# Kernel tuning notes

Hardware: AMD Instinct MI355X
Metric: run time of the kernel (lower is better)

The kernel has to match this reference:

```python
import jax, jax.numpy as jnp
import numpy as np

B, N, C, H = 4, 2048, 768, 12
D = C // H  # 64
EPS = 1e-12


def setup_inputs() -> dict:
    key = jax.random.key(0)
    ks = jax.random.split(key, 8)
    s = 0.02
    return {
        "x": jax.random.normal(ks[0], (B, N, C), dtype=jnp.float32),
        "Wq": jax.random.normal(ks[1], (C, C), dtype=jnp.float32) * s,
        "bq": jnp.zeros((C,), dtype=jnp.float32),
        "Wkv": jax.random.normal(ks[2], (C, 2 * C), dtype=jnp.float32) * s,
        "bkv": jnp.zeros((2 * C,), dtype=jnp.float32),
        "Wproj": jax.random.normal(ks[3], (C, C), dtype=jnp.float32) * s,
        "bproj": jnp.zeros((C,), dtype=jnp.float32),
        "scale": jnp.full((1, H, 1, 1), D ** -0.5, dtype=jnp.float32),
    }


def _l2norm(t):
    # F.normalize(dim=-1): x / max(||x||_2, eps)
    n = jnp.sqrt(jnp.sum(t * t, axis=-1, keepdims=True))
    return t / jnp.maximum(n, EPS)


def reference(x, Wq, bq, Wkv, bkv, Wproj, bproj, scale):
    b, n, c = x.shape
    q = (x @ Wq + bq).reshape(b, n, H, D).transpose(0, 2, 1, 3)        # [B,H,N,D]
    kv = (x @ Wkv + bkv).reshape(b, n, 2, H, D).transpose(2, 0, 3, 1, 4)
    k, v = kv[0], kv[1]                                                # [B,H,N,D]
    q = _l2norm(q)
    k = _l2norm(k)
    attn = jnp.einsum("bhqd,bhkd->bhqk", q, k) * scale                 # [B,H,N,N]
    attn = jax.nn.softmax(attn, axis=-1)
    out = jnp.einsum("bhqk,bhkd->bhqd", attn, v)                       # [B,H,N,D]
    out = out.transpose(0, 2, 1, 3).reshape(b, n, c)
    return out @ Wproj + bproj
```

## Files before the change

kernel.cpp:

```cpp
#include <hip/hip_runtime.h>
#include <hip/hip_bf16.h>
#include <math.h>


typedef short bf16x8 __attribute__((ext_vector_type(8)));
typedef float f32x4 __attribute__((ext_vector_type(4)));
typedef float f32x16 __attribute__((ext_vector_type(16)));

static __device__ __forceinline__ unsigned short f2bf(float f) {
    unsigned int u = __float_as_uint(f);
    unsigned int r = u + 0x7fff + ((u >> 16) & 1);
    return (unsigned short)(r >> 16);
}
static __device__ __forceinline__ unsigned int pack2(float a, float b) {
    return (unsigned int)f2bf(a) | ((unsigned int)f2bf(b) << 16);
}
static __device__ __forceinline__ unsigned int cvtpk(float a, float b) {
    unsigned int r;
    asm("v_cvt_pk_bf16_f32 %0, %1, %2" : "=v"(r) : "v"(a), "v"(b));
    return r;
}
static __device__ __forceinline__ void gl_lds16(const void* g, void* l) {
    __builtin_amdgcn_global_load_lds(
        (const __attribute__((address_space(1))) unsigned int*)g,
        (__attribute__((address_space(3))) unsigned int*)l, 16, 0, 0);
}

__global__ __launch_bounds__(256) void convx_kernel(
    const float* __restrict__ in, unsigned short* __restrict__ out)
{
    size_t i = ((size_t)blockIdx.x * 256 + threadIdx.x) * 8;
    float4 a = *(const float4*)&in[i];
    float4 b = *(const float4*)&in[i + 4];
    uint4 o = make_uint4(pack2(a.x, a.y), pack2(a.z, a.w), pack2(b.x, b.y), pack2(b.z, b.w));
    *(uint4*)&out[i] = o;
}

__global__ __launch_bounds__(256) void convT_kernel(
    const float* __restrict__ Wq, const float* __restrict__ Wkv, const float* __restrict__ Wp,
    unsigned short* __restrict__ WqkvT, unsigned short* __restrict__ WprjT)
{
    __shared__ char tb[8192];
    const int bx = blockIdx.x, k0 = blockIdx.y * 64;
    const float* src; int ld; int cbase; unsigned short* out; int c0;
    if (bx < 36) {
        c0 = bx * 64; out = WqkvT;
        if (c0 < 768) { src = Wq;  ld = 768;  cbase = c0; }
        else          { src = Wkv; ld = 1536; cbase = c0 - 768; }
    } else {
        c0 = (bx - 36) * 64; out = WprjT; src = Wp; ld = 768; cbase = c0;
    }
    const int t = threadIdx.x;
    const int kl = t >> 2, cq = (t & 3) * 16;
    #pragma unroll
    for (int jj = 0; jj < 4; ++jj) {
        float4 v = *(const float4*)&src[(size_t)(k0 + kl) * ld + cbase + cq + jj * 4];
        float vv[4] = {v.x, v.y, v.z, v.w};
        #pragma unroll
        for (int je = 0; je < 4; ++je) {
            int c = cq + jj * 4 + je;
            *(unsigned short*)(tb + c * 128 + ((kl * 2) ^ ((c & 7) << 4))) = f2bf(vv[je]);
        }
    }
    __syncthreads();
    const int cl = t >> 2, u2 = (t & 3) * 2;
    uint4 r0 = *(const uint4*)(tb + cl * 128 + ((u2 ^ (cl & 7)) << 4));
    uint4 r1 = *(const uint4*)(tb + cl * 128 + (((u2 + 1) ^ (cl & 7)) << 4));
    size_t ob = (size_t)(c0 + cl) * 768 + k0 + (t & 3) * 16;
    *(uint4*)&out[ob] = r0;
    *(uint4*)&out[ob + 8] = r1;
}

__global__ __launch_bounds__(256) void qkv_gemm_kernel(
    const unsigned short* __restrict__ xb, const unsigned short* __restrict__ WT,
    const float* __restrict__ bq, const float* __restrict__ bkv,
    const float* __restrict__ scale,
    unsigned short* __restrict__ Qb, unsigned short* __restrict__ Kb,
    unsigned short* __restrict__ Vtb)
{
    __shared__ char lds[32768] __attribute__((aligned(16)));

    const int ct = blockIdx.x;
    const int row0 = blockIdx.y * 128;
    const int tid = threadIdx.x;
    const int w = tid >> 6, l = tid & 63;
    const int g = l >> 4, ln = l & 15;
    const int wr = w >> 1, wc = w & 1;
    const int col0 = ct * 128;

    const int srow = (w & 1) * 64 + (l >> 3);
    const int su = ((l & 7) ^ (l >> 3)) * 16;
    const char* s = (w < 2)
        ? (const char*)xb + (size_t)(row0 + srow) * 1536 + su
        : (const char*)WT + (size_t)(col0 + srow) * 1536 + su;
    char* dbase = lds + ((w >= 2) ? 16384 : 0) + (w & 1) * 8192;

    f32x4 acc[4][4];
    #pragma unroll
    for (int m = 0; m < 4; ++m)
        #pragma unroll
        for (int n = 0; n < 4; ++n) acc[m][n] = (f32x4){0.f, 0.f, 0.f, 0.f};

    const int arow = (wr * 64 + ln) * 128;
    const int brow = 16384 + (wc * 64 + ln) * 128;
    const int x0 = ((0 + g) ^ (ln & 7)) * 16;
    const int x1 = ((4 + g) ^ (ln & 7)) * 16;

    for (int ks = 0; ks < 12; ++ks) {
        __syncthreads();
        #pragma unroll
        for (int j = 0; j < 8; ++j)
            gl_lds16(s + (size_t)j * 8 * 1536, dbase + j * 1024);
        s += 128;
        __syncthreads();
        #pragma unroll
        for (int kc = 0; kc < 2; ++kc) {
            const int xo = kc ? x1 : x0;
            bf16x8 af[4], bfr[4];
            #pragma unroll
            for (int m = 0; m < 4; ++m) af[m] = *(const bf16x8*)(lds + arow + m * 2048 + xo);
            #pragma unroll
            for (int n = 0; n < 4; ++n) bfr[n] = *(const bf16x8*)(lds + brow + n * 2048 + xo);
            #pragma unroll
            for (int m = 0; m < 4; ++m)
                #pragma unroll
                for (int n = 0; n < 4; ++n)
                    acc[m][n] = __builtin_amdgcn_mfma_f32_16x16x32_bf16(af[m], bfr[n], acc[m][n], 0, 0, 0);
        }
    }

    const int co = col0 + wc * 64 + ln;
    float bv[4];
    #pragma unroll
    for (int n = 0; n < 4; ++n) {
        int c = co + n * 16;
        bv[n] = (c < 768) ? bq[c] : bkv[c - 768];
    }
    const int region = ct / 6;
    const int h = (ct % 6) * 2 + wc;

    if (region < 2) {
        unsigned short* dst = (region == 0) ? Qb : Kb;
        const float post = (region == 0) ? scale[0] * 1.4426950408889634f : 1.0f;
        #pragma unroll
        for (int m = 0; m < 4; ++m) {
            #pragma unroll
            for (int n = 0; n < 4; ++n)
                #pragma unroll
                for (int r = 0; r < 4; ++r) acc[m][n][r] += bv[n];
            #pragma unroll
            for (int r = 0; r < 4; ++r) {
                float ss = 0.f;
                #pragma unroll
                for (int n = 0; n < 4; ++n) ss += acc[m][n][r] * acc[m][n][r];
                ss += __shfl_xor(ss, 1); ss += __shfl_xor(ss, 2);
                ss += __shfl_xor(ss, 4); ss += __shfl_xor(ss, 8);
                float inv = post / fmaxf(sqrtf(ss), 1e-12f);
                int t = row0 + wr * 64 + m * 16 + g * 4 + r;
                int b = t >> 11, nt = t & 2047;
                size_t base = ((size_t)(b * 12 + h) * 2048 + nt) * 64 + ln;
                #pragma unroll
                for (int n = 0; n < 4; ++n)
                    dst[base + n * 16] = f2bf(acc[m][n][r] * inv);
            }
        }
    } else {
        char* tb = lds + w * 8192;
        __syncthreads();
        #pragma unroll
        for (int m = 0; m < 4; ++m)
            #pragma unroll
            for (int n = 0; n < 4; ++n)
                #pragma unroll
                for (int r = 0; r < 4; ++r) {
                    int d = n * 16 + ln;
                    int tok = m * 16 + g * 4 + r;
                    *(unsigned short*)(tb + d * 128 + ((tok * 2) ^ ((d & 7) << 4))) =
                        f2bf(acc[m][n][r] + bv[n]);
                }
        __syncthreads();
        const int t0 = row0 + wr * 64;
        const int b = t0 >> 11, n0 = t0 & 2047;
        #pragma unroll
        for (int i = 0; i < 8; ++i) {
            int d = i * 8 + (l >> 3);
            uint4 v = *(const uint4*)(tb + d * 128 + (((l & 7) ^ (d & 7)) << 4));
            *(uint4*)&Vtb[((size_t)(b * 12 + h) * 64 + d) * 2048 + n0 + (l & 7) * 8] = v;
        }
    }
}

__global__ __launch_bounds__(128, 2) void attn_kernel(
    const unsigned short* __restrict__ Qg, const unsigned short* __restrict__ Kg,
    const unsigned short* __restrict__ Vtg,
    unsigned short* __restrict__ O)
{
    __shared__ char lds[32768] __attribute__((aligned(16)));

    const int bid = blockIdx.y * 16 + blockIdx.x;
    const int swzb = (bid & 7) * 96 + (bid >> 3);
    const int bh = swzb >> 4;
    const int q0 = (swzb & 15) * 128;

    const int tid = threadIdx.x;
    const int w  = tid >> 6;
    const int l  = tid & 63;
    const int lo = l & 31;
    const int hi = l >> 5;

    const int srow = w * 32 + (l >> 3);
    const int su   = ((l & 7) ^ (l >> 3)) * 16;
    const char* kS = (const char*)Kg  + ((size_t)bh * 2048 + srow) * 128 + su;
    const char* vS = (const char*)Vtg + ((size_t)bh * 64   + srow) * 4096 + su;
    char* kD = lds + w * 4096;
    char* vD = lds + 16384 + w * 4096;

    auto stage = [&](int t, int buf) {
        const char* pk = kS + (size_t)t * 8192;
        const char* pv = vS + (size_t)t * 128;
        char* dk = kD + buf * 8192;
        char* dv = vD + buf * 8192;
        #pragma unroll
        for (int i = 0; i < 4; ++i) {
            gl_lds16(pk + i * 1024, dk + i * 1024);
            gl_lds16(pv + (size_t)i * 32768, dv + i * 1024);
        }
    };

    bf16x8 qfA[4], qfB[4];
    {
        const unsigned short* qp = Qg + ((size_t)bh * 2048 + q0 + w * 64 + lo) * 64 + hi * 8;
        #pragma unroll
        for (int c = 0; c < 4; ++c) {
            qfA[c] = *(const bf16x8*)(qp + c * 16);
            qfB[c] = *(const bf16x8*)(qp + 2048 + c * 16);
        }
    }

    const int swz = (lo & 7) << 4;
    const int rowb = lo * 128;
    int coff[4];
    #pragma unroll
    for (int c = 0; c < 4; ++c) coff[c] = (c * 32 + hi * 16) ^ swz;

    f32x16 oA0, oA1, oB0, oB1;
    #pragma unroll
    for (int r = 0; r < 16; ++r) { oA0[r] = 0.f; oA1[r] = 0.f; oB0[r] = 0.f; oB1[r] = 0.f; }
    float rsA = 0.f, rsB = 0.f;

    const f32x16 zero16 = {0.f,0.f,0.f,0.f,0.f,0.f,0.f,0.f,0.f,0.f,0.f,0.f,0.f,0.f,0.f,0.f};

    auto compute = [&](const int OFF) {
        const char* Kb = lds + OFF;
        const char* Vb = lds + 16384 + OFF;

        bf16x8 kf[4], kg2[4];
        #pragma unroll
        for (int c = 0; c < 4; ++c) {
            kf[c]  = *(const bf16x8*)(Kb + rowb + coff[c]);
            kg2[c] = *(const bf16x8*)(Kb + 4096 + rowb + coff[c]);
        }

        f32x16 sA0, sA1, sB0, sB1;
        __builtin_amdgcn_s_setprio(1);
        sA0 = __builtin_amdgcn_mfma_f32_32x32x16_bf16(kf[0], qfA[0], zero16, 0, 0, 0);
        sA0 = __builtin_amdgcn_mfma_f32_32x32x16_bf16(kf[1], qfA[1], sA0, 0, 0, 0);
        sA0 = __builtin_amdgcn_mfma_f32_32x32x16_bf16(kf[2], qfA[2], sA0, 0, 0, 0);
        sA0 = __builtin_amdgcn_mfma_f32_32x32x16_bf16(kf[3], qfA[3], sA0, 0, 0, 0);
        sA1 = __builtin_amdgcn_mfma_f32_32x32x16_bf16(kg2[0], qfA[0], zero16, 0, 0, 0);
        sA1 = __builtin_amdgcn_mfma_f32_32x32x16_bf16(kg2[1], qfA[1], sA1, 0, 0, 0);
        sA1 = __builtin_amdgcn_mfma_f32_32x32x16_bf16(kg2[2], qfA[2], sA1, 0, 0, 0);
        sA1 = __builtin_amdgcn_mfma_f32_32x32x16_bf16(kg2[3], qfA[3], sA1, 0, 0, 0);
        sB0 = __builtin_amdgcn_mfma_f32_32x32x16_bf16(kf[0], qfB[0], zero16, 0, 0, 0);
        sB0 = __builtin_amdgcn_mfma_f32_32x32x16_bf16(kf[1], qfB[1], sB0, 0, 0, 0);
        sB0 = __builtin_amdgcn_mfma_f32_32x32x16_bf16(kf[2], qfB[2], sB0, 0, 0, 0);
        sB0 = __builtin_amdgcn_mfma_f32_32x32x16_bf16(kf[3], qfB[3], sB0, 0, 0, 0);
        sB1 = __builtin_amdgcn_mfma_f32_32x32x16_bf16(kg2[0], qfB[0], zero16, 0, 0, 0);
        sB1 = __builtin_amdgcn_mfma_f32_32x32x16_bf16(kg2[1], qfB[1], sB1, 0, 0, 0);
        sB1 = __builtin_amdgcn_mfma_f32_32x32x16_bf16(kg2[2], qfB[2], sB1, 0, 0, 0);
        sB1 = __builtin_amdgcn_mfma_f32_32x32x16_bf16(kg2[3], qfB[3], sB1, 0, 0, 0);
        __builtin_amdgcn_s_setprio(0);

        unsigned int pA[16], pB[16];
        #pragma unroll
        for (int kb = 0; kb < 2; ++kb) {
            float e[16];
            #pragma unroll
            for (int r = 0; r < 16; ++r)
                e[r] = __builtin_amdgcn_exp2f(kb ? sA1[r] : sA0[r]);
            float t = 0.f;
            #pragma unroll
            for (int r = 0; r < 16; r += 4) t += (e[r] + e[r+1]) + (e[r+2] + e[r+3]);
            rsA += t;
            #pragma unroll
            for (int ksb = 0; ksb < 2; ++ksb) {
                pA[kb*8 + ksb*4 + 0] = cvtpk(e[ksb*8 + 0], e[ksb*8 + 1]);
                pA[kb*8 + ksb*4 + 1] = cvtpk(e[ksb*8 + 2], e[ksb*8 + 3]);
                pA[kb*8 + ksb*4 + 2] = cvtpk(e[ksb*8 + 4], e[ksb*8 + 5]);
                pA[kb*8 + ksb*4 + 3] = cvtpk(e[ksb*8 + 6], e[ksb*8 + 7]);
            }
        }
        #pragma unroll
        for (int kb = 0; kb < 2; ++kb) {
            float e[16];
            #pragma unroll
            for (int r = 0; r < 16; ++r)
                e[r] = __builtin_amdgcn_exp2f(kb ? sB1[r] : sB0[r]);
            float t = 0.f;
            #pragma unroll
            for (int r = 0; r < 16; r += 4) t += (e[r] + e[r+1]) + (e[r+2] + e[r+3]);
            rsB += t;
            #pragma unroll
            for (int ksb = 0; ksb < 2; ++ksb) {
                pB[kb*8 + ksb*4 + 0] = cvtpk(e[ksb*8 + 0], e[ksb*8 + 1]);
                pB[kb*8 + ksb*4 + 1] = cvtpk(e[ksb*8 + 2], e[ksb*8 + 3]);
                pB[kb*8 + ksb*4 + 2] = cvtpk(e[ksb*8 + 4], e[ksb*8 + 5]);
                pB[kb*8 + ksb*4 + 3] = cvtpk(e[ksb*8 + 6], e[ksb*8 + 7]);
            }
        }

        #pragma unroll
        for (int kb = 0; kb < 2; ++kb) {
            #pragma unroll
            for (int ksb = 0; ksb < 2; ++ksb) {
                const int base = kb*8 + ksb*4;
                const int ks = kb*2 + ksb;
                bf16x8 v0 = *(const bf16x8*)(Vb + rowb + coff[ks]);
                bf16x8 v1 = *(const bf16x8*)(Vb + 4096 + rowb + coff[ks]);
                unsigned int a0 = pA[base], a1 = pA[base+1], a2 = pA[base+2], a3 = pA[base+3];
                asm("v_permlane32_swap_b32 %0, %1" : "+v"(a0), "+v"(a2));
                asm("v_permlane32_swap_b32 %0, %1" : "+v"(a1), "+v"(a3));
                unsigned int fwA[4] = {a0, a1, a2, a3};
                bf16x8 paA; __builtin_memcpy(&paA, fwA, 16);
                unsigned int b0 = pB[base], b1 = pB[base+1], b2 = pB[base+2], b3 = pB[base+3];
                asm("v_permlane32_swap_b32 %0, %1" : "+v"(b0), "+v"(b2));
                asm("v_permlane32_swap_b32 %0, %1" : "+v"(b1), "+v"(b3));
                unsigned int fwB[4] = {b0, b1, b2, b3};
                bf16x8 paB; __builtin_memcpy(&paB, fwB, 16);
                __builtin_amdgcn_s_setprio(1);
                oA0 = __builtin_amdgcn_mfma_f32_32x32x16_bf16(paA, v0, oA0, 0, 0, 0);
                oA1 = __builtin_amdgcn_mfma_f32_32x32x16_bf16(paA, v1, oA1, 0, 0, 0);
                oB0 = __builtin_amdgcn_mfma_f32_32x32x16_bf16(paB, v0, oB0, 0, 0, 0);
                oB1 = __builtin_amdgcn_mfma_f32_32x32x16_bf16(paB, v1, oB1, 0, 0, 0);
                __builtin_amdgcn_s_setprio(0);
            }
        }
    };

    stage(0, 0);
    __syncthreads();

    #pragma unroll 1
    for (int it = 0; it < 16; ++it) {
        stage(2 * it + 1, 1);
        compute(0);
        __syncthreads();
        if (it < 15) stage(2 * it + 2, 0);
        compute(8192);
        __syncthreads();
    }

    float vA = rsA; vA += __shfl_xor(vA, 32);
    float vB = rsB; vB += __shfl_xor(vB, 32);
    const int b = bh / 12, h = bh % 12;
    #pragma unroll
    for (int r = 0; r < 16; ++r) {
        const int qr = (r & 3) + 8 * (r >> 2) + 4 * hi;
        float invA = 1.0f / __shfl(vA, qr);
        float invB = 1.0f / __shfl(vB, qr);
        size_t baseA = ((size_t)(b * 2048 + q0 + w * 64 + qr)) * 768 + h * 64 + lo;
        O[baseA]      = f2bf(oA0[r] * invA);
        O[baseA + 32] = f2bf(oA1[r] * invA);
        size_t baseB = baseA + (size_t)32 * 768;
        O[baseB]      = f2bf(oB0[r] * invB);
        O[baseB + 32] = f2bf(oB1[r] * invB);
    }
}

__global__ __launch_bounds__(256) void proj_gemm_kernel(
    const unsigned short* __restrict__ Ob, const unsigned short* __restrict__ WT,
    const float* __restrict__ bp, float* __restrict__ out)
{
    __shared__ char lds[32768] __attribute__((aligned(16)));

    const int row0 = blockIdx.y * 128;
    const int col0 = blockIdx.x * 128;
    const int tid = threadIdx.x;
    const int w = tid >> 6, l = tid & 63;
    const int g = l >> 4, ln = l & 15;
    const int wr = w >> 1, wc = w & 1;

    const int srow = (w & 1) * 64 + (l >> 3);
    const int su = ((l & 7) ^ (l >> 3)) * 16;
    const char* s = (w < 2)
        ? (const char*)Ob + (size_t)(row0 + srow) * 1536 + su
        : (const char*)WT + (size_t)(col0 + srow) * 1536 + su;
    char* dbase = lds + ((w >= 2) ? 16384 : 0) + (w & 1) * 8192;

    f32x4 acc[4][4];
    #pragma unroll
    for (int m = 0; m < 4; ++m)
        #pragma unroll
        for (int n = 0; n < 4; ++n) acc[m][n] = (f32x4){0.f, 0.f, 0.f, 0.f};

    const int arow = (wr * 64 + ln) * 128;
    const int brow = 16384 + (wc * 64 + ln) * 128;
    const int x0 = ((0 + g) ^ (ln & 7)) * 16;
    const int x1 = ((4 + g) ^ (ln & 7)) * 16;

    for (int ks = 0; ks < 12; ++ks) {
        __syncthreads();
        #pragma unroll
        for (int j = 0; j < 8; ++j)
            gl_lds16(s + (size_t)j * 8 * 1536, dbase + j * 1024);
        s += 128;
        __syncthreads();
        #pragma unroll
        for (int kc = 0; kc < 2; ++kc) {
            const int xo = kc ? x1 : x0;
            bf16x8 af[4], bfr[4];
            #pragma unroll
            for (int m = 0; m < 4; ++m) af[m] = *(const bf16x8*)(lds + arow + m * 2048 + xo);
            #pragma unroll
            for (int n = 0; n < 4; ++n) bfr[n] = *(const bf16x8*)(lds + brow + n * 2048 + xo);
            #pragma unroll
            for (int m = 0; m < 4; ++m)
                #pragma unroll
                for (int n = 0; n < 4; ++n)
                    acc[m][n] = __builtin_amdgcn_mfma_f32_16x16x32_bf16(af[m], bfr[n], acc[m][n], 0, 0, 0);
        }
    }

    const int co = col0 + wc * 64 + ln;
    float bv[4];
    #pragma unroll
    for (int n = 0; n < 4; ++n) bv[n] = bp[co + n * 16];
    #pragma unroll
    for (int m = 0; m < 4; ++m)
        #pragma unroll
        for (int r = 0; r < 4; ++r) {
            int t = row0 + wr * 64 + m * 16 + g * 4 + r;
            #pragma unroll
            for (int n = 0; n < 4; ++n)
                out[(size_t)t * 768 + co + n * 16] = acc[m][n][r] + bv[n];
        }
}

extern "C" void kernel_launch(void* const* d_in, const int* in_sizes, int n_in,
                              void* d_out, int out_size, void* d_ws, size_t ws_size,
                              hipStream_t stream) {
    const float* x     = (const float*)d_in[0];
    const float* Wq    = (const float*)d_in[1];
    const float* bq    = (const float*)d_in[2];
    const float* Wkv   = (const float*)d_in[3];
    const float* bkv   = (const float*)d_in[4];
    const float* Wp    = (const float*)d_in[5];
    const float* bp    = (const float*)d_in[6];
    const float* scale = (const float*)d_in[7];
    float* out = (float*)d_out;

    unsigned short* ws = (unsigned short*)d_ws;
    const size_t SZ = (size_t)4 * 12 * 2048 * 64;
    unsigned short* xbw   = ws;
    unsigned short* WqkvT = xbw + SZ;
    unsigned short* WprjT = WqkvT + (size_t)2304 * 768;
    unsigned short* Qw    = WprjT + (size_t)768 * 768;
    unsigned short* Kw    = Qw + SZ;
    unsigned short* Vtw   = Kw + SZ;
    unsigned short* Ow    = Vtw + SZ;

    convx_kernel<<<3072, 256, 0, stream>>>(x, xbw);
    convT_kernel<<<dim3(48, 12), 256, 0, stream>>>(Wq, Wkv, Wp, WqkvT, WprjT);
    qkv_gemm_kernel<<<dim3(18, 64), 256, 0, stream>>>(xbw, WqkvT, bq, bkv, scale, Qw, Kw, Vtw);
    attn_kernel<<<dim3(16, 48), 128, 0, stream>>>(Qw, Kw, Vtw, Ow);
    proj_gemm_kernel<<<dim3(6, 64), 256, 0, stream>>>(Ow, WprjT, bp, out);
}
```

Before: 148.5 us.

## Split attention key tiles across two waves per query group with LDS reduction

New measurement: 163.9 us. +10.4%, slower.

```diff
diff --git a/kernel.cpp b/kernel.cpp
--- a/kernel.cpp
+++ b/kernel.cpp
@@ -190,12 +190,12 @@
     }
 }
 
-__global__ __launch_bounds__(128, 2) void attn_kernel(
+__global__ __launch_bounds__(256, 3) void attn_kernel(
     const unsigned short* __restrict__ Qg, const unsigned short* __restrict__ Kg,
     const unsigned short* __restrict__ Vtg,
     unsigned short* __restrict__ O)
 {
-    __shared__ char lds[32768] __attribute__((aligned(16)));
+    __shared__ char lds[35840] __attribute__((aligned(16)));
 
     const int bid = blockIdx.y * 16 + blockIdx.x;
     const int swzb = (bid & 7) * 96 + (bid >> 3);
@@ -207,29 +207,19 @@
     const int l  = tid & 63;
     const int lo = l & 31;
     const int hi = l >> 5;
-
-    const int srow = w * 32 + (l >> 3);
+    const int kh = w & 1;
+    const int qh = w >> 1;
+
+    const int srow = w * 16 + (l >> 3);
     const int su   = ((l & 7) ^ (l >> 3)) * 16;
     const char* kS = (const char*)Kg  + ((size_t)bh * 2048 + srow) * 128 + su;
     const char* vS = (const char*)Vtg + ((size_t)bh * 64   + srow) * 4096 + su;
-    char* kD = lds + w * 4096;
-    char* vD = lds + 16384 + w * 4096;
-
-    auto stage = [&](int t, int buf) {
-        const char* pk = kS + (size_t)t * 8192;
-        const char* pv = vS + (size_t)t * 128;
-        char* dk = kD + buf * 8192;
-        char* dv = vD + buf * 8192;
-        #pragma unroll
-        for (int i = 0; i < 4; ++i) {
-            gl_lds16(pk + i * 1024, dk + i * 1024);
-            gl_lds16(pv + (size_t)i * 32768, dv + i * 1024);
-        }
-    };
+    char* kD = lds + w * 2048;
+    char* vD = lds + 16384 + w * 2048;
 
     bf16x8 qfA[4], qfB[4];
     {
-        const unsigned short* qp = Qg + ((size_t)bh * 2048 + q0 + w * 64 + lo) * 64 + hi * 8;
+        const unsigned short* qp = Qg + ((size_t)bh * 2048 + q0 + qh * 64 + lo) * 64 + hi * 8;
         #pragma unroll
         for (int c = 0; c < 4; ++c) {
             qfA[c] = *(const bf16x8*)(qp + c * 16);
@@ -239,6 +229,7 @@
 
     const int swz = (lo & 7) << 4;
     const int rowb = lo * 128;
+    const int krow = kh * 4096;
     int coff[4];
     #pragma unroll
     for (int c = 0; c < 4; ++c) coff[c] = (c * 32 + hi * 16) ^ swz;
@@ -254,126 +245,150 @@
         const char* Kb = lds + OFF;
         const char* Vb = lds + 16384 + OFF;
 
-        bf16x8 kf[4], kg2[4];
-        #pragma unroll
-        for (int c = 0; c < 4; ++c) {
-            kf[c]  = *(const bf16x8*)(Kb + rowb + coff[c]);
-            kg2[c] = *(const bf16x8*)(Kb + 4096 + rowb + coff[c]);
-        }
-
-        f32x16 sA0, sA1, sB0, sB1;
-        __builtin_amdgcn_s_setprio(1);
-        sA0 = __builtin_amdgcn_mfma_f32_32x32x16_bf16(kf[0], qfA[0], zero16, 0, 0, 0);
-        sA0 = __builtin_amdgcn_mfma_f32_32x32x16_bf16(kf[1], qfA[1], sA0, 0, 0, 0);
-        sA0 = __builtin_amdgcn_mfma_f32_32x32x16_bf16(kf[2], qfA[2], sA0, 0, 0, 0);
-        sA0 = __builtin_amdgcn_mfma_f32_32x32x16_bf16(kf[3], qfA[3], sA0, 0, 0, 0);
-        sA1 = __builtin_amdgcn_mfma_f32_32x32x16_bf16(kg2[0], qfA[0], zero16, 0, 0, 0);
-        sA1 = __builtin_amdgcn_mfma_f32_32x32x16_bf16(kg2[1], qfA[1], sA1, 0, 0, 0);
-        sA1 = __builtin_amdgcn_mfma_f32_32x32x16_bf16(kg2[2], qfA[2], sA1, 0, 0, 0);
-        sA1 = __builtin_amdgcn_mfma_f32_32x32x16_bf16(kg2[3], qfA[3], sA1, 0, 0, 0);
-        sB0 = __builtin_amdgcn_mfma_f32_32x32x16_bf16(kf[0], qfB[0], zero16, 0, 0, 0);
-        sB0 = __builtin_amdgcn_mfma_f32_32x32x16_bf16(kf[1], qfB[1], sB0, 0, 0, 0);
-        sB0 = __builtin_amdgcn_mfma_f32_32x32x16_bf16(kf[2], qfB[2], sB0, 0, 0, 0);
-        sB0 = __builtin_amdgcn_mfma_f32_32x32x16_bf16(kf[3], qfB[3], sB0, 0, 0, 0);
-        sB1 = __builtin_amdgcn_mfma_f32_32x32x16_bf16(kg2[0], qfB[0], zero16, 0, 0, 0);
-        sB1 = __builtin_amdgcn_mfma_f32_32x32x16_bf16(kg2[1], qfB[1], sB1, 0, 0, 0);
-        sB1 = __builtin_amdgcn_mfma_f32_32x32x16_bf16(kg2[2], qfB[2], sB1, 0, 0, 0);
-        sB1 = __builtin_amdgcn_mfma_f32_32x32x16_bf16(kg2[3], qfB[3], sB1, 0, 0, 0);
-        __builtin_amdgcn_s_setprio(0);
-
-        unsigned int pA[16], pB[16];
-        #pragma unroll
-        for (int kb = 0; kb < 2; ++kb) {
+        bf16x8 kf[4];
+        #pragma unroll
+        for (int c = 0; c < 4; ++c)
+            kf[c] = *(const bf16x8*)(Kb + krow + rowb + coff[c]);
+
+        unsigned int pA[8], pB[8];
+        {
+            f32x16 s;
+            __builtin_amdgcn_s_setprio(1);
+            s = __builtin_amdgcn_mfma_f32_32x32x16_bf16(kf[0], qfA[0], zero16, 0, 0, 0);
+            s = __builtin_amdgcn_mfma_f32_32x32x16_bf16(kf[1], qfA[1], s, 0, 0, 0);
+            s = __builtin_amdgcn_mfma_f32_32x32x16_bf16(kf[2], qfA[2], s, 0, 0, 0);
+            s = __builtin_amdgcn_mfma_f32_32x32x16_bf16(kf[3], qfA[3], s, 0, 0, 0);
+            __builtin_amdgcn_s_setprio(0);
             float e[16];
             #pragma unroll
-            for (int r = 0; r < 16; ++r)
-                e[r] = __builtin_amdgcn_exp2f(kb ? sA1[r] : sA0[r]);
+            for (int r = 0; r < 16; ++r) e[r] = __builtin_amdgcn_exp2f(s[r]);
             float t = 0.f;
             #pragma unroll
             for (int r = 0; r < 16; r += 4) t += (e[r] + e[r+1]) + (e[r+2] + e[r+3]);
             rsA += t;
             #pragma unroll
             for (int ksb = 0; ksb < 2; ++ksb) {
-                pA[kb*8 + ksb*4 + 0] = cvtpk(e[ksb*8 + 0], e[ksb*8 + 1]);
-                pA[kb*8 + ksb*4 + 1] = cvtpk(e[ksb*8 + 2], e[ksb*8 + 3]);
-                pA[kb*8 + ksb*4 + 2] = cvtpk(e[ksb*8 + 4], e[ksb*8 + 5]);
-                pA[kb*8 + ksb*4 + 3] = cvtpk(e[ksb*8 + 6], e[ksb*8 + 7]);
+                pA[ksb*4 + 0] = cvtpk(e[ksb*8 + 0], e[ksb*8 + 1]);
+                pA[ksb*4 + 1] = cvtpk(e[ksb*8 + 2], e[ksb*8 + 3]);
+                pA[ksb*4 + 2] = cvtpk(e[ksb*8 + 4], e[ksb*8 + 5]);
+                pA[ksb*4 + 3] = cvtpk(e[ksb*8 + 6], e[ksb*8 + 7]);
             }
         }
-        #pragma unroll
-        for (int kb = 0; kb < 2; ++kb) {
+        {
+            f32x16 s;
+            __builtin_amdgcn_s_setprio(1);
+            s = __builtin_amdgcn_mfma_f32_32x32x16_bf16(kf[0], qfB[0], zero16, 0, 0, 0);
+            s = __builtin_amdgcn_mfma_f32_32x32x16_bf16(kf[1], qfB[1], s, 0, 0, 0);
+            s = __builtin_amdgcn_mfma_f32_32x32x16_bf16(kf[2], qfB[2], s, 0, 0, 0);
+            s = __builtin_amdgcn_mfma_f32_32x32x16_bf16(kf[3], qfB[3], s, 0, 0, 0);
+            __builtin_amdgcn_s_setprio(0);
             float e[16];
             #pragma unroll
-            for (int r = 0; r < 16; ++r)
-                e[r] = __builtin_amdgcn_exp2f(kb ? sB1[r] : sB0[r]);
+            for (int r = 0; r < 16; ++r) e[r] = __builtin_amdgcn_exp2f(s[r]);
             float t = 0.f;
             #pragma unroll
             for (int r = 0; r < 16; r += 4) t += (e[r] + e[r+1]) + (e[r+2] + e[r+3]);
             rsB += t;
             #pragma unroll
             for (int ksb = 0; ksb < 2; ++ksb) {
-                pB[kb*8 + ksb*4 + 0] = cvtpk(e[ksb*8 + 0], e[ksb*8 + 1]);
-                pB[kb*8 + ksb*4 + 1] = cvtpk(e[ksb*8 + 2], e[ksb*8 + 3]);
-                pB[kb*8 + ksb*4 + 2] = cvtpk(e[ksb*8 + 4], e[ksb*8 + 5]);
-                pB[kb*8 + ksb*4 + 3] = cvtpk(e[ksb*8 + 6], e[ksb*8 + 7]);
+                pB[ksb*4 + 0] = cvtpk(e[ksb*8 + 0], e[ksb*8 + 1]);
+                pB[ksb*4 + 1] = cvtpk(e[ksb*8 + 2], e[ksb*8 + 3]);
+                pB[ksb*4 + 2] = cvtpk(e[ksb*8 + 4], e[ksb*8 + 5]);
+                pB[ksb*4 + 3] = cvtpk(e[ksb*8 + 6], e[ksb*8 + 7]);
             }
         }
 
         #pragma unroll
-        for (int kb = 0; kb < 2; ++kb) {
-            #pragma unroll
-            for (int ksb = 0; ksb < 2; ++ksb) {
-                const int base = kb*8 + ksb*4;
-                const int ks = kb*2 + ksb;
-                bf16x8 v0 = *(const bf16x8*)(Vb + rowb + coff[ks]);
-                bf16x8 v1 = *(const bf16x8*)(Vb + 4096 + rowb + coff[ks]);
-                unsigned int a0 = pA[base], a1 = pA[base+1], a2 = pA[base+2], a3 = pA[base+3];
-                asm("v_permlane32_swap_b32 %0, %1" : "+v"(a0), "+v"(a2));
-                asm("v_permlane32_swap_b32 %0, %1" : "+v"(a1), "+v"(a3));
-                unsigned int fwA[4] = {a0, a1, a2, a3};
-                bf16x8 paA; __builtin_memcpy(&paA, fwA, 16);
-                unsigned int b0 = pB[base], b1 = pB[base+1], b2 = pB[base+2], b3 = pB[base+3];
-                asm("v_permlane32_swap_b32 %0, %1" : "+v"(b0), "+v"(b2));
-                asm("v_permlane32_swap_b32 %0, %1" : "+v"(b1), "+v"(b3));
-                unsigned int fwB[4] = {b0, b1, b2, b3};
-                bf16x8 paB; __builtin_memcpy(&paB, fwB, 16);
-                __builtin_amdgcn_s_setprio(1);
-                oA0 = __builtin_amdgcn_mfma_f32_32x32x16_bf16(paA, v0, oA0, 0, 0, 0);
-                oA1 = __builtin_amdgcn_mfma_f32_32x32x16_bf16(paA, v1, oA1, 0, 0, 0);
-                oB0 = __builtin_amdgcn_mfma_f32_32x32x16_bf16(paB, v0, oB0, 0, 0, 0);
-                oB1 = __builtin_amdgcn_mfma_f32_32x32x16_bf16(paB, v1, oB1, 0, 0, 0);
-                __builtin_amdgcn_s_setprio(0);
-            }
+        for (int ksb = 0; ksb < 2; ++ksb) {
+            const int gks = kh * 2 + ksb;
+            bf16x8 v0 = *(const bf16x8*)(Vb + rowb + coff[gks]);
+            bf16x8 v1 = *(const bf16x8*)(Vb + 4096 + rowb + coff[gks]);
+            unsigned int a0 = pA[ksb*4 + 0], a1 = pA[ksb*4 + 1];
+            unsigned int a2 = pA[ksb*4 + 2], a3 = pA[ksb*4 + 3];
+            asm("v_permlane32_swap_b32 %0, %1" : "+v"(a0), "+v"(a2));
+            asm("v_permlane32_swap_b32 %0, %1" : "+v"(a1), "+v"(a3));
+            unsigned int fwA[4] = {a0, a1, a2, a3};
+            bf16x8 paA; __builtin_memcpy(&paA, fwA, 16);
+            unsigned int b0 = pB[ksb*4 + 0], b1 = pB[ksb*4 + 1];
+            unsigned int b2 = pB[ksb*4 + 2], b3 = pB[ksb*4 + 3];
+            asm("v_permlane32_swap_b32 %0, %1" : "+v"(b0), "+v"(b2));
+            asm("v_permlane32_swap_b32 %0, %1" : "+v"(b1), "+v"(b3));
+            unsigned int fwB[4] = {b0, b1, b2, b3};
+            bf16x8 paB; __builtin_memcpy(&paB, fwB, 16);
+            __builtin_amdgcn_s_setprio(1);
+            oA0 = __builtin_amdgcn_mfma_f32_32x32x16_bf16(paA, v0, oA0, 0, 0, 0);
+            oA1 = __builtin_amdgcn_mfma_f32_32x32x16_bf16(paA, v1, oA1, 0, 0, 0);
+            oB0 = __builtin_amdgcn_mfma_f32_32x32x16_bf16(paB, v0, oB0, 0, 0, 0);
+            oB1 = __builtin_amdgcn_mfma_f32_32x32x16_bf16(paB, v1, oB1, 0, 0, 0);
+            __builtin_amdgcn_s_setprio(0);
         }
     };
 
-    stage(0, 0);
+    gl_lds16(kS, kD);          gl_lds16(kS + 1024, kD + 1024);
+    gl_lds16(vS, vD);          gl_lds16(vS + 32768, vD + 1024);
+    kS += 8192; vS += 128;
     __syncthreads();
 
     #pragma unroll 1
     for (int it = 0; it < 16; ++it) {
-        stage(2 * it + 1, 1);
+        gl_lds16(kS, kD + 8192);          gl_lds16(kS + 1024, kD + 9216);
+        gl_lds16(vS, vD + 8192);          gl_lds16(vS + 32768, vD + 9216);
+        kS += 8192; vS += 128;
         compute(0);
         __syncthreads();
-        if (it < 15) stage(2 * it + 2, 0);
+        if (it < 15) {
+            gl_lds16(kS, kD);          gl_lds16(kS + 1024, kD + 1024);
+            gl_lds16(vS, vD);          gl_lds16(vS + 32768, vD + 1024);
+            kS += 8192; vS += 128;
+        }
         compute(8192);
         __syncthreads();
     }
 
-    float vA = rsA; vA += __shfl_xor(vA, 32);
-    float vB = rsB; vB += __shfl_xor(vB, 32);
-    const int b = bh / 12, h = bh % 12;
-    #pragma unroll
-    for (int r = 0; r < 16; ++r) {
-        const int qr = (r & 3) + 8 * (r >> 2) + 4 * hi;
-        float invA = 1.0f / __shfl(vA, qr);
-        float invB = 1.0f / __shfl(vB, qr);
-        size_t baseA = ((size_t)(b * 2048 + q0 + w * 64 + qr)) * 768 + h * 64 + lo;
-        O[baseA]      = f2bf(oA0[r] * invA);
-        O[baseA + 32] = f2bf(oA1[r] * invA);
-        size_t baseB = baseA + (size_t)32 * 768;
-        O[baseB]      = f2bf(oB0[r] * invB);
-        O[baseB + 32] = f2bf(oB1[r] * invB);
+    rsA += __shfl_xor(rsA, 32);
+    rsB += __shfl_xor(rsB, 32);
+
+    float* obuf  = (float*)lds;
+    float* rsbuf = (float*)(lds + 34816);
+
+    if (kh == 1) {
+        float* dst = obuf + qh * 4352 + l * 68;
+        #pragma unroll
+        for (int i = 0; i < 4; ++i) {
+            *(f32x4*)(dst + i * 4)      = (f32x4){oA0[i*4], oA0[i*4+1], oA0[i*4+2], oA0[i*4+3]};
+            *(f32x4*)(dst + 16 + i * 4) = (f32x4){oA1[i*4], oA1[i*4+1], oA1[i*4+2], oA1[i*4+3]};
+            *(f32x4*)(dst + 32 + i * 4) = (f32x4){oB0[i*4], oB0[i*4+1], oB0[i*4+2], oB0[i*4+3]};
+            *(f32x4*)(dst + 48 + i * 4) = (f32x4){oB1[i*4], oB1[i*4+1], oB1[i*4+2], oB1[i*4+3]};
+        }
+        rsbuf[qh * 128 + l]      = rsA;
+        rsbuf[qh * 128 + 64 + l] = rsB;
+    }
+    __syncthreads();
+    if (kh == 0) {
+        const float* src = obuf + qh * 4352 + l * 68;
+        #pragma unroll
+        for (int i = 0; i < 16; ++i) {
+            oA0[i] += src[i];
+            oA1[i] += src[16 + i];
+            oB0[i] += src[32 + i];
+            oB1[i] += src[48 + i];
+        }
+        rsA += rsbuf[qh * 128 + l];
+        rsB += rsbuf[qh * 128 + 64 + l];
+
+        const int b = bh / 12, h = bh % 12;
+        #pragma unroll
+        for (int r = 0; r < 16; ++r) {
+            const int qr = (r & 3) + 8 * (r >> 2) + 4 * hi;
+            float invA = 1.0f / __shfl(rsA, qr);
+            float invB = 1.0f / __shfl(rsB, qr);
+            size_t baseA = ((size_t)(b * 2048 + q0 + qh * 64 + qr)) * 768 + h * 64 + lo;
+            O[baseA]      = f2bf(oA0[r] * invA);
+            O[baseA + 32] = f2bf(oA1[r] * invA);
+            size_t baseB = baseA + (size_t)32 * 768;
+            O[baseB]      = f2bf(oB0[r] * invB);
+            O[baseB + 32] = f2bf(oB1[r] * invB);
+        }
     }
 }
 
@@ -472,6 +487,6 @@
     convx_kernel<<<3072, 256, 0, stream>>>(x, xbw);
     convT_kernel<<<dim3(48, 12), 256, 0, stream>>>(Wq, Wkv, Wp, WqkvT, WprjT);
     qkv_gemm_kernel<<<dim3(18, 64), 256, 0, stream>>>(xbw, WqkvT, bq, bkv, scale, Qw, Kw, Vtw);
-    attn_kernel<<<dim3(16, 48), 128, 0, stream>>>(Qw, Kw, Vtw, Ow);
+    attn_kernel<<<dim3(16, 48), 256, 0, stream>>>(Qw, Kw, Vtw, Ow);
     proj_gemm_kernel<<<dim3(6, 64), 256, 0, stream>>>(Ow, WprjT, bp, out);
 }
```
